# Performance work log

Measured on AMD Instinct MI355X. Metric: run time of the kernel, lower is better.

Reference implementation:

```python
import jax, jax.numpy as jnp
import numpy as np

N = 65536      # collocation points
HID = 256      # hidden_dim
D = 3          # input_dim (x, y, t)
O = 2          # output_dim (streamfunction s, pressure p)


def _xavier(k, shape):
    fan_out, fan_in = shape
    std = (2.0 / (fan_in + fan_out)) ** 0.5
    return std * jax.random.normal(k, shape, dtype=jnp.float32)


def setup_inputs() -> dict:
    key = jax.random.key(0)
    ks = jax.random.split(key, 16)
    z = lambda n: jnp.zeros((n,), dtype=jnp.float32)
    return {
        "x": jax.random.normal(ks[0], (N,), dtype=jnp.float32),
        "y": jax.random.normal(ks[1], (N,), dtype=jnp.float32),
        "t": jax.random.normal(ks[2], (N,), dtype=jnp.float32),
        "p": jax.random.normal(ks[3], (N,), dtype=jnp.float32),
        "u": jax.random.normal(ks[4], (N,), dtype=jnp.float32),
        "v": jax.random.normal(ks[5], (N,), dtype=jnp.float32),
        # shared trunk: 3 Linear+Tanh layers
        "W1": _xavier(ks[6], (HID, D)),   "b1": z(HID),
        "W2": _xavier(ks[7], (HID, HID)), "b2": z(HID),
        "W3": _xavier(ks[8], (HID, HID)), "b3": z(HID),
        # pde head
        "Wp1": _xavier(ks[9], (HID, HID)),  "bp1": z(HID),
        "Wp2": _xavier(ks[10], (O, HID)),   "bp2": z(O),
        # data head
        "Wd1": _xavier(ks[11], (HID, HID)), "bd1": z(HID),
        "Wd2": _xavier(ks[12], (O, HID)),   "bd2": z(O),
        "lam1": jnp.float32(1.0),
        "lam2": jnp.float32(0.2),
    }


def reference(x, y, t, p, u, v,
              W1, b1, W2, b2, W3, b3,
              Wp1, bp1, Wp2, bp2,
              Wd1, bd1, Wd2, bd2,
              lam1, lam2):
    def trunk(q):  # q: [3]
        h = jnp.tanh(W1 @ q + b1)
        h = jnp.tanh(W2 @ h + b2)
        h = jnp.tanh(W3 @ h + b3)
        return h

    def pde_out(q):
        return Wp2 @ jnp.tanh(Wp1 @ trunk(q) + bp1) + bp2  # [2]

    def data_out(q):
        return Wd2 @ jnp.tanh(Wd1 @ trunk(q) + bd1) + bd2  # [2]

    s_pde = lambda q: pde_out(q)[0]
    p_pde = lambda q: pde_out(q)[1]
    s_data = lambda q: data_out(q)[0]

    grad_s = jax.grad(s_pde)                 # [3]  (s_x, s_y, s_t)
    hess_s = jax.jacfwd(grad_s)              # [3,3]
    third_s = jax.jacfwd(hess_s)             # [3,3,3]

    def per_sample(q):
        g1 = grad_s(q)
        H2 = hess_s(q)
        T3 = third_s(q)
        gp = jax.grad(p_pde)(q)
        do = data_out(q)
        gsd = jax.grad(s_data)(q)

        u_ = g1[1]            # u = ds/dy
        v_ = -g1[0]           # v = -ds/dx
        u_x, u_y, u_t = H2[1, 0], H2[1, 1], H2[1, 2]
        v_x, v_y, v_t = -H2[0, 0], -H2[0, 1], -H2[0, 2]
        u_xx, u_yy = T3[1, 0, 0], T3[1, 1, 1]
        v_xx, v_yy = -T3[0, 0, 0], -T3[0, 1, 1]
        p_x, p_y = gp[0], gp[1]

        f_ = lam1 * (u_t + u_ * u_x + v_ * u_y) + p_x - lam2 * (u_xx + u_yy)
        g_ = lam1 * (v_t + u_ * v_x + v_ * v_y) + p_y - lam2 * (v_xx + v_yy)

        p_pred = do[1]        # data head pressure
        u_pred = gsd[1]       # d s_data / dy
        v_pred = -gsd[0]      # -d s_data / dx
        return p_pred, u_pred, v_pred, f_, g_

    q = jnp.stack([x, y, t], axis=1)  # [N, 3]
    p_pred, u_pred, v_pred, f_, g_ = jax.vmap(per_sample)(q)
    return p_pred, u_pred, v_pred, f_, g_
```

## Files before the change

kernel.cpp:

```cpp
#include <hip/hip_runtime.h>


#define N_PTS 65536
#define HID   256
#define TS    6
#define MROWS (TS * 13)
#define MT    5

typedef _Float16 half_t;
typedef __attribute__((ext_vector_type(8))) _Float16 half8;
typedef __attribute__((ext_vector_type(4))) float floatx4;

#define J_HI   0
#define REDBUF 39936
#define LDS_BYTES (REDBUF + 288)

struct alignas(4) hpair { half_t a, b; };

__device__ __forceinline__ float fast_tanh(float x) {
    float e = __builtin_amdgcn_exp2f(x * 2.885390081777927f);
    return 1.f - 2.f * __builtin_amdgcn_rcpf(e + 1.f);
}

__device__ __forceinline__ void tanh_jet(const float* u, float* h) {
    const float f  = fast_tanh(u[0]);
    const float f1 = 1.f - f * f;
    const float f2 = -2.f * f * f1;
    const float f3 = -2.f * f1 * f1 + 4.f * f * f * f1;
    const float ux = u[1], uy = u[2], ut = u[3];
    const float uxx = u[4], uxy = u[5], uyy = u[6], uxt = u[7], uyt = u[8];
    h[0] = f;
    h[1] = f1 * ux;  h[2] = f1 * uy;  h[3] = f1 * ut;
    h[4] = f2 * ux * ux + f1 * uxx;
    h[5] = f2 * ux * uy + f1 * uxy;
    h[6] = f2 * uy * uy + f1 * uyy;
    h[7] = f2 * ux * ut + f1 * uxt;
    h[8] = f2 * uy * ut + f1 * uyt;
    h[9]  = f3 * ux * ux * ux + 3.f * f2 * ux * uxx + f1 * u[9];
    h[10] = f3 * ux * ux * uy + f2 * (uxx * uy + 2.f * uxy * ux) + f1 * u[10];
    h[11] = f3 * ux * uy * uy + f2 * (uyy * ux + 2.f * uxy * uy) + f1 * u[11];
    h[12] = f3 * uy * uy * uy + 3.f * f2 * uy * uyy + f1 * u[12];
}

__global__ void prep_w(const float* __restrict__ W2, const float* __restrict__ W3,
                       const float* __restrict__ Wp1, const float* __restrict__ Wd1,
                       half_t* __restrict__ ws) {
    int idx = blockIdx.x * 256 + threadIdx.x;
#pragma unroll
    for (int r = 0; r < 4; ++r) {
        int e = idx + r * 65536;
        int m = e >> 16, i = e & 65535;
        const float* src = (m == 0) ? W2 : (m == 1) ? W3 : (m == 2) ? Wp1 : Wd1;
        float w = src[i];
        half_t hi = (half_t)w;
        half_t lo = (half_t)(w - (float)hi);
        int n = i >> 8, k = i & 255;
        int addr = (((n >> 4) * 8 + (k >> 5)) * 64 + ((k >> 3) & 3) * 16 + (n & 15)) * 8
                   + (k & 7);
        ws[m * 131072 + addr] = hi;
        ws[m * 131072 + 65536 + addr] = lo;
    }
}

__device__ __forceinline__ void load_B(const half_t* bh, int vo, int kb,
                                       half8 (&Bh)[4]) {
#pragma unroll
    for (int nt = 0; nt < 4; ++nt) {
        int off = nt * 4096 + kb * 512 + vo;
        Bh[nt] = *(const half8*)(bh + off);
    }
}

__device__ __forceinline__ void mfma_phase(const char* __restrict__ smem,
                                           const int (&mx)[MT], const int (&mr)[MT],
                                           int kb, int q,
                                           const half8 (&Bh)[4],
                                           floatx4 (&acc)[MT][4]) {
    const int kq = (kb * 4 + q) << 4;
    __builtin_amdgcn_s_setprio(1);
#pragma unroll
    for (int mt = 0; mt < MT; ++mt) {
        const int a = mr[mt] + (kq ^ mx[mt]);
        half8 Ah = *(const half8*)(smem + J_HI + a);
#pragma unroll
        for (int nt = 0; nt < 4; ++nt) {
            acc[mt][nt] = __builtin_amdgcn_mfma_f32_16x16x32_f16(Ah, Bh[nt], acc[mt][nt], 0, 0, 0);
        }
    }
    __builtin_amdgcn_s_setprio(0);
}

__device__ __forceinline__ void epi_pre(const float* __restrict__ bias,
                                        int wave, int lane,
                                        floatx4 (&acc)[MT][4], float (&ho)[MROWS]) {
    const int n = wave * 64 + lane;
    const float bn = bias[n];
    float col[MT * 16];
    const int s_lo[MT] = {0, 1, 2, 3, 4};
    const int s_hi[MT] = {0, 1, 2, 3, 5};
#pragma unroll
    for (int mt = 0; mt < MT; ++mt) {
        float tv[4][4];
#pragma unroll
        for (int j = 0; j < 4; ++j)
#pragma unroll
            for (int r = 0; r < 4; ++r) tv[j][r] = acc[mt][j][r];
#pragma unroll
        for (int r = 0; r < 4; ++r) {
            asm("v_permlane16_swap_b32 %0, %1" : "+v"(tv[0][r]), "+v"(tv[1][r]));
            asm("v_permlane16_swap_b32 %0, %1" : "+v"(tv[2][r]), "+v"(tv[3][r]));
            asm("v_permlane32_swap_b32 %0, %1" : "+v"(tv[0][r]), "+v"(tv[2][r]));
            asm("v_permlane32_swap_b32 %0, %1" : "+v"(tv[1][r]), "+v"(tv[3][r]));
        }
#pragma unroll
        for (int j = 0; j < 4; ++j)
#pragma unroll
            for (int r = 0; r < 4; ++r) col[mt * 16 + j * 4 + r] = tv[j][r];
#pragma unroll
        for (int s = s_lo[mt]; s <= s_hi[mt]; ++s) {
            float u[13], htmp[13];
#pragma unroll
            for (int c = 0; c < 13; ++c) u[c] = col[s * 13 + c];
            u[0] += bn;
            tanh_jet(u, htmp);
#pragma unroll
            for (int c = 0; c < 13; ++c) ho[s * 13 + c] = htmp[c];
        }
    }
}

__device__ __forceinline__ void epi_post(char* __restrict__ smem, int wave, int lane,
                                         const float (&ho)[MROWS]) {
    const int n = wave * 64 + lane;
    const int lanebase = ((n >> 3) << 4) | ((n & 7) << 1);
#pragma unroll
    for (int m = 0; m < MROWS; ++m) {
        const int off = m * 512 + (lanebase ^ ((m & 15) << 4));
        *(half_t*)(smem + J_HI + off) = (half_t)ho[m];
    }
}

__device__ __forceinline__ void layer(char* __restrict__ smem,
                                      const half_t* bh,
                                      const float* __restrict__ bias,
                                      int wave, int lane, int vo, int q, int nl,
                                      const half_t* nbh,
                                      half8 (&P0h)[4],
                                      floatx4 (&acc)[MT][4]) {
    int mx[MT], mr[MT];
#pragma unroll
    for (int mt = 0; mt < MT; ++mt) {
        int m = mt * 16 + nl;
        if (m > MROWS - 1) m = MROWS - 1;
        mx[mt] = (m & 15) << 4;
        mr[mt] = m * 512;
    }
    half8 B1h[4], B2h[4];
    load_B(bh, vo, 1, B1h);
#pragma unroll
    for (int mt = 0; mt < MT; ++mt)
#pragma unroll
        for (int nt = 0; nt < 4; ++nt) acc[mt][nt] = floatx4{0.f, 0.f, 0.f, 0.f};
    mfma_phase(smem, mx, mr, 0, q, P0h, acc);
    load_B(bh, vo, 2, B2h);
    mfma_phase(smem, mx, mr, 1, q, B1h, acc);
#pragma unroll 1
    for (int kb = 2; kb < 8; kb += 2) {
        load_B(bh, vo, kb + 1, B1h);
        mfma_phase(smem, mx, mr, kb, q, B2h, acc);
        if (kb + 2 < 8) load_B(bh, vo, kb + 2, B2h);
        mfma_phase(smem, mx, mr, kb + 1, q, B1h, acc);
    }
    load_B(nbh, vo, 0, P0h);
    float ho[MROWS];
    epi_pre(bias, wave, lane, acc, ho);
    __syncthreads();
    epi_post(smem, wave, lane, ho);
    __syncthreads();
}

__device__ __forceinline__ void head_phase(const char* __restrict__ smem,
                                           const int (&mh)[2], int kb, int q,
                                           const half8 (&Bh)[4],
                                           floatx4 (&hacc)[2][4]) {
    __builtin_amdgcn_s_setprio(1);
#pragma unroll
    for (int ht = 0; ht < 2; ++ht) {
        const int a = mh[ht] * 512 + ((((kb * 4 + q) << 4)) ^ ((mh[ht] & 15) << 4));
        half8 Ah = *(const half8*)(smem + J_HI + a);
#pragma unroll
        for (int nt = 0; nt < 4; ++nt) {
            hacc[ht][nt] = __builtin_amdgcn_mfma_f32_16x16x32_f16(Ah, Bh[nt], hacc[ht][nt], 0, 0, 0);
        }
    }
    __builtin_amdgcn_s_setprio(0);
}

__global__ __launch_bounds__(256, 2) void pinn_mfma(
    const float* __restrict__ gx, const float* __restrict__ gy, const float* __restrict__ gt,
    const float* __restrict__ W1, const float* __restrict__ b1,
    const float* __restrict__ b2, const float* __restrict__ b3,
    const float* __restrict__ bp1, const float* __restrict__ Wp2,
    const float* __restrict__ bd1, const float* __restrict__ Wd2,
    const float* __restrict__ bd2,
    const float* __restrict__ lam1p, const float* __restrict__ lam2p,
    const half_t* __restrict__ wsw, float* __restrict__ out) {
    extern __shared__ char smem[];
    const int t = threadIdx.x;
    const int wave = t >> 6, lane = t & 63;
    const int q = lane >> 4, nl = lane & 15;
    const int base = blockIdx.x * TS;
    const int wo = __builtin_amdgcn_readfirstlane(wave) * 16384;
    const int vo = lane * 8;

    const half_t* W2h = wsw + wo;
    const half_t* W3h = wsw + 131072 + wo;
    const half_t* Wph = wsw + 2 * 131072 + wo;
    const half_t* Wdh = wsw + 3 * 131072 + wo;

    half8 P0h[4];
    load_B(W2h, vo, 0, P0h);

#pragma unroll 1
    for (int ii = 0; ii < 3; ++ii) {
        int p = ii * 256 + t;
        int s = p >> 7, j = (p & 127) * 2;
        int gi = base + s; if (gi >= N_PTS) gi = N_PTS - 1;
        float qx = gx[gi], qy = gy[gi], qt = gt[gi];
        float hv[2][13];
#pragma unroll
        for (int d = 0; d < 2; ++d) {
            int jj = j + d;
            float w0 = W1[3 * jj], w1 = W1[3 * jj + 1], w2 = W1[3 * jj + 2];
            float f = fast_tanh(w0 * qx + w1 * qy + w2 * qt + b1[jj]);
            float f1 = 1.f - f * f;
            float f2c = -2.f * f * f1;
            float f3c = -2.f * f1 * f1 + 4.f * f * f * f1;
            float* h = hv[d];
            h[0] = f; h[1] = f1 * w0; h[2] = f1 * w1; h[3] = f1 * w2;
            h[4] = f2c * w0 * w0; h[5] = f2c * w0 * w1; h[6] = f2c * w1 * w1;
            h[7] = f2c * w0 * w2; h[8] = f2c * w1 * w2;
            h[9]  = f3c * w0 * w0 * w0; h[10] = f3c * w0 * w0 * w1;
            h[11] = f3c * w0 * w1 * w1; h[12] = f3c * w1 * w1 * w1;
        }
#pragma unroll
        for (int c = 0; c < 13; ++c) {
            int m = s * 13 + c;
            int off = m * 512 + ((((j) >> 3) ^ (m & 15)) << 4) + ((j & 7) << 1);
            half_t hA = (half_t)hv[0][c], hB = (half_t)hv[1][c];
            *(hpair*)(smem + J_HI + off) = hpair{hA, hB};
        }
    }
    __syncthreads();

    floatx4 acc[MT][4];

    layer(smem, W2h, b2, wave, lane, vo, q, nl, W3h, P0h, acc);
    layer(smem, W3h, b3, wave, lane, vo, q, nl, Wdh, P0h, acc);

    {
        int ch = (nl & 3) == 3 ? 0 : (nl & 3);
        int mh[2];
        mh[0] = (nl >> 2) * 13 + ch;
        {
            int s1 = 4 + (nl >> 2);
            mh[1] = (s1 < TS) ? s1 * 13 + ch : 52;
        }
        floatx4 hacc[2][4];
#pragma unroll
        for (int ht = 0; ht < 2; ++ht)
#pragma unroll
            for (int nt = 0; nt < 4; ++nt) hacc[ht][nt] = floatx4{0.f, 0.f, 0.f, 0.f};
        head_phase(smem, mh, 0, q, P0h, hacc);
#pragma unroll 1
        for (int kb = 1; kb < 8; ++kb) {
            half8 Bh[4];
            load_B(Wdh, vo, kb, Bh);
            head_phase(smem, mh, kb, q, Bh, hacc);
        }
        load_B(Wph, vo, 0, P0h);
        float* rb = (float*)(smem + REDBUF);
#pragma unroll
        for (int ht = 0; ht < 2; ++ht) {
            float pp = 0, up = 0, vp = 0;
#pragma unroll
            for (int nt = 0; nt < 4; ++nt) {
                int n = wave * 64 + nt * 16 + nl;
                floatx4 a = hacc[ht][nt];
                float f = fast_tanh(a.x + bd1[n]);
                float f1 = 1.f - f * f;
                float hdx = f1 * a.y, hdy = f1 * a.z;
                float w0 = Wd2[n], w1 = Wd2[HID + n];
                pp += w1 * f;
                up += w0 * hdy;
                vp -= w0 * hdx;
            }
#pragma unroll
            for (int msk = 1; msk < 16; msk <<= 1) {
                pp += __shfl_xor(pp, msk, 64);
                up += __shfl_xor(up, msk, 64);
                vp += __shfl_xor(vp, msk, 64);
            }
            int s = ht * 4 + q;
            if (nl == 0 && s < TS) {
                rb[(s * 4 + wave) * 3 + 0] = pp;
                rb[(s * 4 + wave) * 3 + 1] = up;
                rb[(s * 4 + wave) * 3 + 2] = vp;
            }
        }
        __syncthreads();
        if (t < TS && base + t < N_PTS) {
            float P = 0, U = 0, V = 0;
#pragma unroll
            for (int w = 0; w < 4; ++w) {
                P += rb[(t * 4 + w) * 3 + 0];
                U += rb[(t * 4 + w) * 3 + 1];
                V += rb[(t * 4 + w) * 3 + 2];
            }
            out[0 * N_PTS + base + t] = P + bd2[1];
            out[1 * N_PTS + base + t] = U;
            out[2 * N_PTS + base + t] = V;
        }
    }

    layer(smem, Wph, bp1, wave, lane, vo, q, nl, Wdh, P0h, acc);

    {
        int s = t >> 5, gl = t & 31;
        if (s < TS) {
            floatx4 w0a = *(const floatx4*)(Wp2 + gl * 8);
            floatx4 w0b = *(const floatx4*)(Wp2 + gl * 8 + 4);
            floatx4 w1a = *(const floatx4*)(Wp2 + HID + gl * 8);
            floatx4 w1b = *(const floatx4*)(Wp2 + HID + gl * 8 + 4);
            float wr0[8] = {w0a.x, w0a.y, w0a.z, w0a.w, w0b.x, w0b.y, w0b.z, w0b.w};
            float wr1[8] = {w1a.x, w1a.y, w1a.z, w1a.w, w1b.x, w1b.y, w1b.z, w1b.w};
            float S[13], px = 0.f, py = 0.f;
#pragma unroll
            for (int c = 0; c < 13; ++c) {
                const int m = s * 13 + c;
                const int off = m * 512 + ((gl ^ (m & 15)) << 4);
                half8 hv = *(const half8*)(smem + J_HI + off);
                float p = 0.f, p2 = 0.f;
#pragma unroll
                for (int e = 0; e < 8; ++e) {
                    float val = (float)hv[e];
                    p += val * wr0[e];
                    if (c == 1 || c == 2) p2 += val * wr1[e];
                }
#pragma unroll
                for (int msk = 1; msk < 32; msk <<= 1) p += __shfl_xor(p, msk, 64);
                S[c] = p;
                if (c == 1) {
#pragma unroll
                    for (int msk = 1; msk < 32; msk <<= 1) p2 += __shfl_xor(p2, msk, 64);
                    px = p2;
                } else if (c == 2) {
#pragma unroll
                    for (int msk = 1; msk < 32; msk <<= 1) p2 += __shfl_xor(p2, msk, 64);
                    py = p2;
                }
            }
            if (gl == 0 && base + s < N_PTS) {
                const float lam1 = lam1p[0], lam2 = lam2p[0];
                const float u_ = S[2], v_ = -S[1];
                const float u_x = S[5], u_y = S[6], u_t = S[8];
                const float v_x = -S[4], v_y = -S[5], v_t = -S[7];
                const float u_xx = S[10], u_yy = S[12];
                const float v_xx = -S[9], v_yy = -S[11];
                const float f_ = lam1 * (u_t + u_ * u_x + v_ * u_y) + px - lam2 * (u_xx + u_yy);
                const float g_ = lam1 * (v_t + u_ * v_x + v_ * v_y) + py - lam2 * (v_xx + v_yy);
                out[3 * N_PTS + base + s] = f_;
                out[4 * N_PTS + base + s] = g_;
            }
        }
    }
}

extern "C" void kernel_launch(void* const* d_in, const int* in_sizes, int n_in,
                              void* d_out, int out_size, void* d_ws, size_t ws_size,
                              hipStream_t stream) {
    const float* x   = (const float*)d_in[0];
    const float* y   = (const float*)d_in[1];
    const float* tt  = (const float*)d_in[2];
    const float* W1  = (const float*)d_in[6];
    const float* b1  = (const float*)d_in[7];
    const float* W2  = (const float*)d_in[8];
    const float* b2  = (const float*)d_in[9];
    const float* W3  = (const float*)d_in[10];
    const float* b3  = (const float*)d_in[11];
    const float* Wp1 = (const float*)d_in[12];
    const float* bp1 = (const float*)d_in[13];
    const float* Wp2 = (const float*)d_in[14];
    const float* Wd1 = (const float*)d_in[16];
    const float* bd1 = (const float*)d_in[17];
    const float* Wd2 = (const float*)d_in[18];
    const float* bd2 = (const float*)d_in[19];
    const float* l1  = (const float*)d_in[20];
    const float* l2  = (const float*)d_in[21];
    float* out = (float*)d_out;
    half_t* wsw = (half_t*)d_ws;

    prep_w<<<256, 256, 0, stream>>>(W2, W3, Wp1, Wd1, wsw);

    (void)hipFuncSetAttribute((const void*)pinn_mfma,
                              hipFuncAttributeMaxDynamicSharedMemorySize,
                              (int)LDS_BYTES);
    pinn_mfma<<<(N_PTS + TS - 1) / TS, 256, LDS_BYTES, stream>>>(
        x, y, tt, W1, b1, b2, b3, bp1, Wp2, bd1, Wd2, bd2, l1, l2, wsw, out);
}
```

Baseline: 556.3 us.

## Interleave data-head and PDE-head MFMA passes with double-buffered weight loads

The data-head k-loop and the separate PDE-head layer now run together in one unrolled k-loop. Each step issues a data-head MFMA phase and a PDE-head MFMA phase over the same shared-memory activations, and the next weight fragments are prefetched into alternating register buffers. This removes the second sweep over the LDS activations, a separate layer call and its barrier, and hides global weight-load latency behind compute. In exchange it raises register pressure (extra accumulator and B buffers, a ho[MROWS] array), which may lower occupancy, and it adds an extra __syncthreads.

```diff
diff --git a/kernel.cpp b/kernel.cpp
--- a/kernel.cpp
+++ b/kernel.cpp
@@ -259,6 +259,14 @@
     layer(smem, W3h, b3, wave, lane, vo, q, nl, Wdh, P0h, acc);
 
     {
+        int mx[MT], mr[MT];
+#pragma unroll
+        for (int mt = 0; mt < MT; ++mt) {
+            int m = mt * 16 + nl;
+            if (m > MROWS - 1) m = MROWS - 1;
+            mx[mt] = (m & 15) << 4;
+            mr[mt] = m * 512;
+        }
         int ch = (nl & 3) == 3 ? 0 : (nl & 3);
         int mh[2];
         mh[0] = (nl >> 2) * 13 + ch;
@@ -271,14 +279,39 @@
         for (int ht = 0; ht < 2; ++ht)
 #pragma unroll
             for (int nt = 0; nt < 4; ++nt) hacc[ht][nt] = floatx4{0.f, 0.f, 0.f, 0.f};
+#pragma unroll
+        for (int mt = 0; mt < MT; ++mt)
+#pragma unroll
+            for (int nt = 0; nt < 4; ++nt) acc[mt][nt] = floatx4{0.f, 0.f, 0.f, 0.f};
+
+        half8 D1[4], Pp0[4], Pp1[4];
+        load_B(Wph, vo, 0, Pp0);
+        load_B(Wdh, vo, 1, D1);
+        load_B(Wph, vo, 1, Pp1);
+
         head_phase(smem, mh, 0, q, P0h, hacc);
-#pragma unroll 1
-        for (int kb = 1; kb < 8; ++kb) {
-            half8 Bh[4];
-            load_B(Wdh, vo, kb, Bh);
-            head_phase(smem, mh, kb, q, Bh, hacc);
-        }
-        load_B(Wph, vo, 0, P0h);
+        mfma_phase(smem, mx, mr, 0, q, Pp0, acc);
+        load_B(Wdh, vo, 2, P0h);  load_B(Wph, vo, 2, Pp0);
+        head_phase(smem, mh, 1, q, D1, hacc);
+        mfma_phase(smem, mx, mr, 1, q, Pp1, acc);
+        load_B(Wdh, vo, 3, D1);   load_B(Wph, vo, 3, Pp1);
+        head_phase(smem, mh, 2, q, P0h, hacc);
+        mfma_phase(smem, mx, mr, 2, q, Pp0, acc);
+        load_B(Wdh, vo, 4, P0h);  load_B(Wph, vo, 4, Pp0);
+        head_phase(smem, mh, 3, q, D1, hacc);
+        mfma_phase(smem, mx, mr, 3, q, Pp1, acc);
+        load_B(Wdh, vo, 5, D1);   load_B(Wph, vo, 5, Pp1);
+        head_phase(smem, mh, 4, q, P0h, hacc);
+        mfma_phase(smem, mx, mr, 4, q, Pp0, acc);
+        load_B(Wdh, vo, 6, P0h);  load_B(Wph, vo, 6, Pp0);
+        head_phase(smem, mh, 5, q, D1, hacc);
+        mfma_phase(smem, mx, mr, 5, q, Pp1, acc);
+        load_B(Wdh, vo, 7, D1);   load_B(Wph, vo, 7, Pp1);
+        head_phase(smem, mh, 6, q, P0h, hacc);
+        mfma_phase(smem, mx, mr, 6, q, Pp0, acc);
+        head_phase(smem, mh, 7, q, D1, hacc);
+        mfma_phase(smem, mx, mr, 7, q, Pp1, acc);
+
         float* rb = (float*)(smem + REDBUF);
 #pragma unroll
         for (int ht = 0; ht < 2; ++ht) {
@@ -308,7 +341,10 @@
                 rb[(s * 4 + wave) * 3 + 2] = vp;
             }
         }
+        float ho[MROWS];
+        epi_pre(bp1, wave, lane, acc, ho);
         __syncthreads();
+        epi_post(smem, wave, lane, ho);
         if (t < TS && base + t < N_PTS) {
             float P = 0, U = 0, V = 0;
 #pragma unroll
@@ -321,9 +357,8 @@
             out[1 * N_PTS + base + t] = U;
             out[2 * N_PTS + base + t] = V;
         }
-    }
-
-    layer(smem, Wph, bp1, wave, lane, vo, q, nl, Wdh, P0h, acc);
+        __syncthreads();
+    }
 
     {
         int s = t >> 5, gl = t & 31;
```

After: 574.4 us. 1.03x slower.
